# Kernel tuning notes

Hardware: AMD Instinct MI355X
Metric: run time of the kernel (lower is better)

The kernel has to match this reference:

```python
import jax, jax.numpy as jnp
import numpy as np

B, S, D = 2048, 8, 1280
K = 1                 # n_components_remove
HIGH_T = 0.6          # PC1_HIGH_ACTIVITY_THRESHOLD
STORM_T = 0.8         # solar_storm_threshold


def setup_inputs() -> dict:
    key = jax.random.key(0)
    k1, k2 = jax.random.split(key, 2)
    features = jax.random.normal(k1, (B, S, D), dtype=jnp.float32)
    kp_index = jax.random.uniform(k2, (B,), dtype=jnp.float32) * 9.0
    cmr_gate = jnp.ones((1,), dtype=jnp.float32)  # nn.Parameter(torch.ones(1))
    return {"features": features, "kp_index": kp_index, "cmr_gate": cmr_gate}


def reference(features, kp_index, cmr_gate):
    # Per-sample standardization over the feature axis (numpy std, ddof=0)
    mu = features.mean(axis=2, keepdims=True)            # (B, S, 1)
    sigma = features.std(axis=2, keepdims=True) + 1e-8   # (B, S, 1)
    fn = (features - mu) / sigma                         # (B, S, D)

    # Batched thin SVD of the (S, D) normalized feature matrix
    U, sv, Vt = jnp.linalg.svd(fn, full_matrices=False)  # (B,S,S), (B,S), (B,S,D)
    var = sv * sv
    pc1_ratio = var[:, 0] / (var.sum(axis=-1) + 1e-8)    # (B,)

    # solar_flag: 0 normal, 1 high activity, 2 storm
    solar_flag = (pc1_ratio >= HIGH_T).astype(jnp.int32) + (pc1_ratio >= STORM_T).astype(jnp.int32)

    # Rank-K reconstruction of the common-mode (solar) component
    low = jnp.einsum('bsk,bk,bkd->bsd', U[:, :, :K], sv[:, :K], Vt[:, :K, :])
    clean = (fn - low) * sigma + mu                      # de-normalized cleaned features

    # Kp-gating: amplify CMR when Kp >= 5
    kp_gate = 1.0 + 0.5 * (kp_index >= 5.0).astype(features.dtype)[:, None, None]
    clean = features + kp_gate * (clean - features)

    # Learnable gate
    gate = jax.nn.sigmoid(cmr_gate)[0]
    features_clean = features + gate * (clean - features)
    return features_clean, pc1_ratio, solar_flag
```

## Files before the change

### kernel.cpp

```cpp
#include <hip/hip_runtime.h>
#include <math.h>


#define SV 8
#define DV 1280
#define BSTRIDE (SV*DV)
#define WSS 17

__global__ __launch_bounds__(256)
void cmr_stats_kernel(const float* __restrict__ feat,
                      const float* __restrict__ kp,
                      const float* __restrict__ cmr_gate,
                      float* __restrict__ cws,
                      float* __restrict__ out,
                      int Bn)
{
    const int lane = threadIdx.x & 63;
    const int b = blockIdx.x * 4 + (threadIdx.x >> 6);

    const float* __restrict__ fb = feat + (size_t)b * BSTRIDE;

    float Sr[8], C[36];
#pragma unroll
    for (int s = 0; s < 8; ++s) Sr[s] = 0.f;
#pragma unroll
    for (int t = 0; t < 36; ++t) C[t] = 0.f;

#pragma unroll
    for (int k = 0; k < DV / 64; ++k) {
        const int d = lane + 64 * k;
        float f[8];
#pragma unroll
        for (int s = 0; s < 8; ++s) f[s] = fb[s * DV + d];
#pragma unroll
        for (int s = 0; s < 8; ++s) Sr[s] += f[s];
        int idx = 0;
#pragma unroll
        for (int i = 0; i < 8; ++i)
#pragma unroll
            for (int j = i; j < 8; ++j) { C[idx] = fmaf(f[i], f[j], C[idx]); ++idx; }
    }
#pragma unroll
    for (int m = 32; m >= 1; m >>= 1) {
#pragma unroll
        for (int s = 0; s < 8; ++s) Sr[s] += __shfl_xor(Sr[s], m);
#pragma unroll
        for (int t = 0; t < 36; ++t) C[t] += __shfl_xor(C[t], m);
    }

    const int i = lane >> 3, j = lane & 7;
    const int a_ = (i < j) ? i : j;
    const int b_ = (i < j) ? j : i;
    const int tii = 8 * i - (i * (i - 1)) / 2;
    const int tjj = 8 * j - (j * (j - 1)) / 2;
    const int tij = 8 * a_ - (a_ * (a_ - 1)) / 2 + (b_ - a_);

    float Ci = 0.f, Cj = 0.f, Cij = 0.f, Si = 0.f, Sj = 0.f;
#pragma unroll
    for (int t = 0; t < 36; ++t) {
        Ci  = (t == tii) ? C[t] : Ci;
        Cj  = (t == tjj) ? C[t] : Cj;
        Cij = (t == tij) ? C[t] : Cij;
    }
#pragma unroll
    for (int s = 0; s < 8; ++s) {
        Si = (s == i) ? Sr[s] : Si;
        Sj = (s == j) ? Sr[s] : Sj;
    }
    const float invD = 1.f / (float)DV;
    const float mui = Si * invD, muj = Sj * invD;
    const float vari = fmaxf(Ci * invD - mui * mui, 0.f);
    const float varj = fmaxf(Cj * invD - muj * muj, 0.f);
    const float sigi = sqrtf(vari) + 1e-8f;
    const float sigj = sqrtf(varj) + 1e-8f;
    const float rsigi = 1.f / sigi, rsigj = 1.f / sigj;
    const float G = ((Cij - (float)DV * mui * muj) * rsigi) * rsigj;

    float tr = (i == j) ? G : 0.f;
#pragma unroll
    for (int m = 32; m >= 1; m >>= 1) tr += __shfl_xor(tr, m);
    const float trs = fmaxf(tr, 1e-30f);

    float A = G / trs;
#pragma unroll
    for (int t = 0; t < 14; ++t) {
        float nb = 0.f;
#pragma unroll
        for (int k = 0; k < 8; ++k)
            nb = fmaf(__shfl(A, i * 8 + k), __shfl(A, k * 8 + j), nb);
        float dg = (i == j) ? nb : 0.f;
#pragma unroll
        for (int m = 32; m >= 1; m >>= 1) dg += __shfl_xor(dg, m);
        A = nb / fmaxf(dg, 1e-30f);
    }

    float dv = (i == j) ? A : -1.f;
    int bj = j;
#pragma unroll
    for (int m = 32; m >= 1; m >>= 1) {
        float ov = __shfl_xor(dv, m);
        int   oj = __shfl_xor(bj, m);
        if (ov > dv) { dv = ov; bj = oj; }
    }
    float u = __shfl(A, i * 8 + bj);
    {
        float nn = (j == 0) ? u * u : 0.f;
#pragma unroll
        for (int m = 32; m >= 1; m >>= 1) nn += __shfl_xor(nn, m);
        u *= rsqrtf(fmaxf(nn, 1e-30f));
    }
#pragma unroll
    for (int it = 0; it < 2; ++it) {
        float y = G * __shfl(u, j * 8);
#pragma unroll
        for (int m = 1; m <= 4; m <<= 1) y += __shfl_xor(y, m);
        float ny = (j == 0) ? y * y : 0.f;
#pragma unroll
        for (int m = 32; m >= 1; m >>= 1) ny += __shfl_xor(ny, m);
        u = y * rsqrtf(fmaxf(ny, 1e-30f));
    }
    float lp = G * u * __shfl(u, j * 8);
#pragma unroll
    for (int m = 32; m >= 1; m >>= 1) lp += __shfl_xor(lp, m);
    const float pc1 = lp / (tr + 1e-8f);

    const float gate = 1.f / (1.f + expf(-cmr_gate[0]));
    const float kpg  = (kp[b] >= 5.0f) ? 1.5f : 1.0f;
    const float Gt   = gate * kpg;

    float bcp = (j == 0) ? u * rsigi * mui : 0.f;
#pragma unroll
    for (int m = 32; m >= 1; m >>= 1) bcp += __shfl_xor(bcp, m);

    float* wsb = cws + (size_t)b * WSS;
    if (j == 0) {
        wsb[i]     = u * rsigi;
        wsb[8 + i] = Gt * sigi * u;
    }
    if (lane == 0) {
        wsb[16] = bcp;
        out[(size_t)Bn * BSTRIDE + b] = pc1;
        const float flag = (pc1 >= 0.6f ? 1.f : 0.f) + (pc1 >= 0.8f ? 1.f : 0.f);
        out[(size_t)Bn * BSTRIDE + Bn + b] = flag;
    }
}

__global__ __launch_bounds__(256)
void cmr_apply_kernel(const float* __restrict__ feat,
                      const float* __restrict__ cws,
                      float* __restrict__ out)
{
    const int lane = threadIdx.x & 63;
    const int b = blockIdx.x * 4 + (threadIdx.x >> 6);

    const float* __restrict__ wsb = cws + (size_t)b * WSS;
    float a[8], c[8];
#pragma unroll
    for (int s = 0; s < 8; ++s) { a[s] = wsb[s]; c[s] = wsb[8 + s]; }
    const float bc = wsb[16];

    const float4* __restrict__ f4 = (const float4*)(feat + (size_t)b * BSTRIDE);
    float4* __restrict__ o4 = (float4*)(out + (size_t)b * BSTRIDE);

#pragma unroll
    for (int k = 0; k < 5; ++k) {
        const int d4 = lane + 64 * k;
        float4 f[8];
#pragma unroll
        for (int s = 0; s < 8; ++s) f[s] = f4[s * (DV / 4) + d4];
        float4 p = make_float4(-bc, -bc, -bc, -bc);
#pragma unroll
        for (int s = 0; s < 8; ++s) {
            p.x = fmaf(a[s], f[s].x, p.x);
            p.y = fmaf(a[s], f[s].y, p.y);
            p.z = fmaf(a[s], f[s].z, p.z);
            p.w = fmaf(a[s], f[s].w, p.w);
        }
#pragma unroll
        for (int s = 0; s < 8; ++s) {
            float4 o;
            o.x = fmaf(-c[s], p.x, f[s].x);
            o.y = fmaf(-c[s], p.y, f[s].y);
            o.z = fmaf(-c[s], p.z, f[s].z);
            o.w = fmaf(-c[s], p.w, f[s].w);
            o4[s * (DV / 4) + d4] = o;
        }
    }
}

extern "C" void kernel_launch(void* const* d_in, const int* in_sizes, int n_in,
                              void* d_out, int out_size, void* d_ws, size_t ws_size,
                              hipStream_t stream) {
    const float* feat = (const float*)d_in[0];
    const float* kp   = (const float*)d_in[1];
    const float* gate = (const float*)d_in[2];
    float* out = (float*)d_out;
    float* cws = (float*)d_ws;
    const int Bn = in_sizes[0] / BSTRIDE;

    cmr_stats_kernel<<<Bn / 4, 256, 0, stream>>>(feat, kp, gate, cws, out, Bn);
    cmr_apply_kernel<<<Bn / 4, 256, 0, stream>>>(feat, cws, out);
}
```

Measured before the change: 179.8 us.

## Fuse stats and apply kernels, keeping each sample's features in registers

Merges the statistics and apply kernels into one kernel. Each wavefront loads its whole 8x1280 sample as float4 into registers (160 floats per lane), computes the Gram/power-iteration statistics, then applies the rank-1 removal from those same registers. This drops the second global read of the features and the workspace round trip. In exchange, register pressure is very high (launch_bounds 256,2), which can cause spills and lowers occupancy, so there is less latency hiding during the single big load phase.

```diff
diff --git a/kernel.cpp b/kernel.cpp
--- a/kernel.cpp
+++ b/kernel.cpp
@@ -4,41 +4,47 @@
 
 #define SV 8
 #define DV 1280
+#define D4 (DV/4)
 #define BSTRIDE (SV*DV)
-#define WSS 17
 
-__global__ __launch_bounds__(256)
-void cmr_stats_kernel(const float* __restrict__ feat,
+__global__ __launch_bounds__(256, 2)
+void cmr_fused_kernel(const float* __restrict__ feat,
                       const float* __restrict__ kp,
                       const float* __restrict__ cmr_gate,
-                      float* __restrict__ cws,
                       float* __restrict__ out,
                       int Bn)
 {
     const int lane = threadIdx.x & 63;
     const int b = blockIdx.x * 4 + (threadIdx.x >> 6);
 
-    const float* __restrict__ fb = feat + (size_t)b * BSTRIDE;
+    const float4* __restrict__ f4 = (const float4*)(feat + (size_t)b * BSTRIDE);
+    float4 f[8][5];
+#pragma unroll
+    for (int k = 0; k < 5; ++k) {
+        const int d4 = lane + 64 * k;
+#pragma unroll
+        for (int s = 0; s < 8; ++s) f[s][k] = f4[s * D4 + d4];
+    }
 
     float Sr[8], C[36];
 #pragma unroll
     for (int s = 0; s < 8; ++s) Sr[s] = 0.f;
 #pragma unroll
     for (int t = 0; t < 36; ++t) C[t] = 0.f;
-
 #pragma unroll
-    for (int k = 0; k < DV / 64; ++k) {
-        const int d = lane + 64 * k;
-        float f[8];
+    for (int k = 0; k < 5; ++k) {
 #pragma unroll
-        for (int s = 0; s < 8; ++s) f[s] = fb[s * DV + d];
-#pragma unroll
-        for (int s = 0; s < 8; ++s) Sr[s] += f[s];
+        for (int s = 0; s < 8; ++s)
+            Sr[s] += (f[s][k].x + f[s][k].y) + (f[s][k].z + f[s][k].w);
         int idx = 0;
 #pragma unroll
         for (int i = 0; i < 8; ++i)
 #pragma unroll
-            for (int j = i; j < 8; ++j) { C[idx] = fmaf(f[i], f[j], C[idx]); ++idx; }
+            for (int j = i; j < 8; ++j) {
+                float t0 = fmaf(f[i][k].x, f[j][k].x, fmaf(f[i][k].y, f[j][k].y, 0.f));
+                float t1 = fmaf(f[i][k].z, f[j][k].z, fmaf(f[i][k].w, f[j][k].w, t0));
+                C[idx] += t1; ++idx;
+            }
     }
 #pragma unroll
     for (int m = 32; m >= 1; m >>= 1) {
@@ -72,8 +78,8 @@
     const float vari = fmaxf(Ci * invD - mui * mui, 0.f);
     const float varj = fmaxf(Cj * invD - muj * muj, 0.f);
     const float sigi = sqrtf(vari) + 1e-8f;
-    const float sigj = sqrtf(varj) + 1e-8f;
-    const float rsigi = 1.f / sigi, rsigj = 1.f / sigj;
+    const float rsigi = 1.f / sigi;
+    const float rsigj = 1.f / (sqrtf(varj) + 1e-8f);
     const float G = ((Cij - (float)DV * mui * muj) * rsigi) * rsigj;
 
     float tr = (i == j) ? G : 0.f;
@@ -93,7 +99,6 @@
         for (int m = 32; m >= 1; m >>= 1) dg += __shfl_xor(dg, m);
         A = nb / fmaxf(dg, 1e-30f);
     }
-
     float dv = (i == j) ? A : -1.f;
     int bj = j;
 #pragma unroll
@@ -128,63 +133,46 @@
     const float kpg  = (kp[b] >= 5.0f) ? 1.5f : 1.0f;
     const float Gt   = gate * kpg;
 
-    float bcp = (j == 0) ? u * rsigi * mui : 0.f;
+    float bc = (j == 0) ? u * rsigi * mui : 0.f;
 #pragma unroll
-    for (int m = 32; m >= 1; m >>= 1) bcp += __shfl_xor(bcp, m);
+    for (int m = 32; m >= 1; m >>= 1) bc += __shfl_xor(bc, m);
 
-    float* wsb = cws + (size_t)b * WSS;
-    if (j == 0) {
-        wsb[i]     = u * rsigi;
-        wsb[8 + i] = Gt * sigi * u;
-    }
-    if (lane == 0) {
-        wsb[16] = bcp;
-        out[(size_t)Bn * BSTRIDE + b] = pc1;
-        const float flag = (pc1 >= 0.6f ? 1.f : 0.f) + (pc1 >= 0.8f ? 1.f : 0.f);
-        out[(size_t)Bn * BSTRIDE + Bn + b] = flag;
-    }
-}
-
-__global__ __launch_bounds__(256)
-void cmr_apply_kernel(const float* __restrict__ feat,
-                      const float* __restrict__ cws,
-                      float* __restrict__ out)
-{
-    const int lane = threadIdx.x & 63;
-    const int b = blockIdx.x * 4 + (threadIdx.x >> 6);
-
-    const float* __restrict__ wsb = cws + (size_t)b * WSS;
+    const float av = u * rsigi;
+    const float cv = Gt * sigi * u;
     float a[8], c[8];
 #pragma unroll
-    for (int s = 0; s < 8; ++s) { a[s] = wsb[s]; c[s] = wsb[8 + s]; }
-    const float bc = wsb[16];
+    for (int s = 0; s < 8; ++s) {
+        a[s] = __shfl(av, s * 8);
+        c[s] = __shfl(cv, s * 8);
+    }
 
-    const float4* __restrict__ f4 = (const float4*)(feat + (size_t)b * BSTRIDE);
     float4* __restrict__ o4 = (float4*)(out + (size_t)b * BSTRIDE);
-
 #pragma unroll
     for (int k = 0; k < 5; ++k) {
         const int d4 = lane + 64 * k;
-        float4 f[8];
-#pragma unroll
-        for (int s = 0; s < 8; ++s) f[s] = f4[s * (DV / 4) + d4];
         float4 p = make_float4(-bc, -bc, -bc, -bc);
 #pragma unroll
         for (int s = 0; s < 8; ++s) {
-            p.x = fmaf(a[s], f[s].x, p.x);
-            p.y = fmaf(a[s], f[s].y, p.y);
-            p.z = fmaf(a[s], f[s].z, p.z);
-            p.w = fmaf(a[s], f[s].w, p.w);
+            p.x = fmaf(a[s], f[s][k].x, p.x);
+            p.y = fmaf(a[s], f[s][k].y, p.y);
+            p.z = fmaf(a[s], f[s][k].z, p.z);
+            p.w = fmaf(a[s], f[s][k].w, p.w);
         }
 #pragma unroll
         for (int s = 0; s < 8; ++s) {
             float4 o;
-            o.x = fmaf(-c[s], p.x, f[s].x);
-            o.y = fmaf(-c[s], p.y, f[s].y);
-            o.z = fmaf(-c[s], p.z, f[s].z);
-            o.w = fmaf(-c[s], p.w, f[s].w);
-            o4[s * (DV / 4) + d4] = o;
+            o.x = fmaf(-c[s], p.x, f[s][k].x);
+            o.y = fmaf(-c[s], p.y, f[s][k].y);
+            o.z = fmaf(-c[s], p.z, f[s][k].z);
+            o.w = fmaf(-c[s], p.w, f[s][k].w);
+            o4[s * D4 + d4] = o;
         }
+    }
+
+    if (lane == 0) {
+        out[(size_t)Bn * BSTRIDE + b] = pc1;
+        const float flag = (pc1 >= 0.6f ? 1.f : 0.f) + (pc1 >= 0.8f ? 1.f : 0.f);
+        out[(size_t)Bn * BSTRIDE + Bn + b] = flag;
     }
 }
 
@@ -194,10 +182,6 @@
     const float* feat = (const float*)d_in[0];
     const float* kp   = (const float*)d_in[1];
     const float* gate = (const float*)d_in[2];
-    float* out = (float*)d_out;
-    float* cws = (float*)d_ws;
     const int Bn = in_sizes[0] / BSTRIDE;
-
-    cmr_stats_kernel<<<Bn / 4, 256, 0, stream>>>(feat, kp, gate, cws, out, Bn);
-    cmr_apply_kernel<<<Bn / 4, 256, 0, stream>>>(feat, cws, out);
+    cmr_fused_kernel<<<Bn / 4, 256, 0, stream>>>(feat, kp, gate, (float*)d_out, Bn);
 }
```

Measured after the change: 249.0 us. +38.4%, slower.

## Use one 320-thread block per sample with LDS cross-wave Gram reduction

Applied to the files above, without the earlier changes.

Both kernels now map one block of five waves to each batch sample instead of one wave per sample. In the stats kernel each thread loads float4s once, computes partial sums and Gram entries, reduces within 8-lane groups, and combines the 40 partials through shared memory. Wave 0 then does the power-iteration eigensolve, with the wide butterfly reductions replaced by direct diagonal-lane shuffles. The aim is more memory-level parallelism and vectorized loads in the bandwidth-bound stats pass, at the cost of a block barrier and four of the five waves sitting idle during the eigen step.

```diff
diff --git a/kernel.cpp b/kernel.cpp
--- a/kernel.cpp
+++ b/kernel.cpp
@@ -4,48 +4,75 @@
 
 #define SV 8
 #define DV 1280
+#define D4 320
 #define BSTRIDE (SV*DV)
+#define LDW 44
 #define WSS 17
 
-__global__ __launch_bounds__(256)
-void cmr_stats_kernel(const float* __restrict__ feat,
-                      const float* __restrict__ kp,
-                      const float* __restrict__ cmr_gate,
-                      float* __restrict__ cws,
-                      float* __restrict__ out,
-                      int Bn)
+__global__ __launch_bounds__(320)
+void cmr_stats(const float* __restrict__ feat,
+               const float* __restrict__ kp,
+               const float* __restrict__ cmr_gate,
+               float* __restrict__ cws,
+               float* __restrict__ out,
+               int Bn)
 {
-    const int lane = threadIdx.x & 63;
-    const int b = blockIdx.x * 4 + (threadIdx.x >> 6);
-
-    const float* __restrict__ fb = feat + (size_t)b * BSTRIDE;
+    __shared__ float lds[44 * LDW];
+    const int tid  = threadIdx.x;
+    const int lane = tid & 63;
+    const int wq   = tid >> 6;
+    const int b    = blockIdx.x;
+
+    const float4* __restrict__ f4 = (const float4*)(feat + (size_t)b * BSTRIDE);
+    const int d4 = wq * 64 + lane;
+    float4 f[8];
+#pragma unroll
+    for (int s = 0; s < 8; ++s) f[s] = f4[s * D4 + d4];
 
     float Sr[8], C[36];
 #pragma unroll
-    for (int s = 0; s < 8; ++s) Sr[s] = 0.f;
-#pragma unroll
-    for (int t = 0; t < 36; ++t) C[t] = 0.f;
-
-#pragma unroll
-    for (int k = 0; k < DV / 64; ++k) {
-        const int d = lane + 64 * k;
-        float f[8];
-#pragma unroll
-        for (int s = 0; s < 8; ++s) f[s] = fb[s * DV + d];
-#pragma unroll
-        for (int s = 0; s < 8; ++s) Sr[s] += f[s];
+    for (int s = 0; s < 8; ++s) Sr[s] = (f[s].x + f[s].y) + (f[s].z + f[s].w);
+    {
         int idx = 0;
 #pragma unroll
-        for (int i = 0; i < 8; ++i)
-#pragma unroll
-            for (int j = i; j < 8; ++j) { C[idx] = fmaf(f[i], f[j], C[idx]); ++idx; }
-    }
-#pragma unroll
-    for (int m = 32; m >= 1; m >>= 1) {
+        for (int i2 = 0; i2 < 8; ++i2)
+#pragma unroll
+            for (int j2 = i2; j2 < 8; ++j2) {
+                float t0 = fmaf(f[i2].x, f[j2].x, fmaf(f[i2].y, f[j2].y, 0.f));
+                C[idx] = fmaf(f[i2].z, f[j2].z, fmaf(f[i2].w, f[j2].w, t0));
+                ++idx;
+            }
+    }
+#pragma unroll
+    for (int m = 1; m <= 4; m <<= 1) {
 #pragma unroll
         for (int s = 0; s < 8; ++s) Sr[s] += __shfl_xor(Sr[s], m);
 #pragma unroll
         for (int t = 0; t < 36; ++t) C[t] += __shfl_xor(C[t], m);
+    }
+    {
+        const int p = wq * 8 + (lane >> 3);
+        if ((lane & 7) == 0) {
+#pragma unroll
+            for (int t = 0; t < 36; ++t) lds[t * LDW + p] = C[t];
+#pragma unroll
+            for (int s = 0; s < 8; ++s) lds[(36 + s) * LDW + p] = Sr[s];
+        }
+    }
+    __syncthreads();
+    if (wq != 0) return;
+
+    float tot;
+    {
+        const float4* l4 = (const float4*)lds;
+        const int Lr = (lane < 44) ? lane : 0;
+        float4 a4 = make_float4(0.f, 0.f, 0.f, 0.f);
+#pragma unroll
+        for (int q = 0; q < 10; ++q) {
+            float4 v = l4[Lr * (LDW / 4) + q];
+            a4.x += v.x; a4.y += v.y; a4.z += v.z; a4.w += v.w;
+        }
+        tot = (a4.x + a4.y) + (a4.z + a4.w);
     }
 
     const int i = lane >> 3, j = lane & 7;
@@ -54,83 +81,75 @@
     const int tii = 8 * i - (i * (i - 1)) / 2;
     const int tjj = 8 * j - (j * (j - 1)) / 2;
     const int tij = 8 * a_ - (a_ * (a_ - 1)) / 2 + (b_ - a_);
-
-    float Ci = 0.f, Cj = 0.f, Cij = 0.f, Si = 0.f, Sj = 0.f;
-#pragma unroll
-    for (int t = 0; t < 36; ++t) {
-        Ci  = (t == tii) ? C[t] : Ci;
-        Cj  = (t == tjj) ? C[t] : Cj;
-        Cij = (t == tij) ? C[t] : Cij;
-    }
-#pragma unroll
-    for (int s = 0; s < 8; ++s) {
-        Si = (s == i) ? Sr[s] : Si;
-        Sj = (s == j) ? Sr[s] : Sj;
-    }
+    const float Cij = __shfl(tot, tij);
+    const float Ci  = __shfl(tot, tii);
+    const float Cj  = __shfl(tot, tjj);
+    const float Si  = __shfl(tot, 36 + i);
+    const float Sj  = __shfl(tot, 36 + j);
+
     const float invD = 1.f / (float)DV;
     const float mui = Si * invD, muj = Sj * invD;
     const float vari = fmaxf(Ci * invD - mui * mui, 0.f);
     const float varj = fmaxf(Cj * invD - muj * muj, 0.f);
-    const float sigi = sqrtf(vari) + 1e-8f;
-    const float sigj = sqrtf(varj) + 1e-8f;
-    const float rsigi = 1.f / sigi, rsigj = 1.f / sigj;
+    const float sigi  = sqrtf(vari) + 1e-8f;
+    const float rsigi = 1.f / sigi;
+    const float rsigj = 1.f / (sqrtf(varj) + 1e-8f);
     const float G = ((Cij - (float)DV * mui * muj) * rsigi) * rsigj;
 
-    float tr = (i == j) ? G : 0.f;
-#pragma unroll
-    for (int m = 32; m >= 1; m >>= 1) tr += __shfl_xor(tr, m);
-    const float trs = fmaxf(tr, 1e-30f);
-
-    float A = G / trs;
+    float tr = 0.f;
+#pragma unroll
+    for (int k = 0; k < 8; ++k) tr += __shfl(G, 9 * k);
+
+    float A = G / fmaxf(tr, 1e-30f);
 #pragma unroll
     for (int t = 0; t < 14; ++t) {
         float nb = 0.f;
 #pragma unroll
         for (int k = 0; k < 8; ++k)
             nb = fmaf(__shfl(A, i * 8 + k), __shfl(A, k * 8 + j), nb);
-        float dg = (i == j) ? nb : 0.f;
-#pragma unroll
-        for (int m = 32; m >= 1; m >>= 1) dg += __shfl_xor(dg, m);
+        float dg = 0.f;
+#pragma unroll
+        for (int k = 0; k < 8; ++k) dg += __shfl(nb, 9 * k);
         A = nb / fmaxf(dg, 1e-30f);
     }
-
-    float dv = (i == j) ? A : -1.f;
-    int bj = j;
-#pragma unroll
-    for (int m = 32; m >= 1; m >>= 1) {
-        float ov = __shfl_xor(dv, m);
-        int   oj = __shfl_xor(bj, m);
-        if (ov > dv) { dv = ov; bj = oj; }
+    float best = __shfl(A, 0); int bj = 0;
+#pragma unroll
+    for (int k = 1; k < 8; ++k) {
+        float dk = __shfl(A, 9 * k);
+        if (dk > best) { best = dk; bj = k; }
     }
     float u = __shfl(A, i * 8 + bj);
     {
-        float nn = (j == 0) ? u * u : 0.f;
-#pragma unroll
-        for (int m = 32; m >= 1; m >>= 1) nn += __shfl_xor(nn, m);
+        float nn = 0.f;
+#pragma unroll
+        for (int k = 0; k < 8; ++k) nn += __shfl(u * u, 9 * k);
         u *= rsqrtf(fmaxf(nn, 1e-30f));
     }
 #pragma unroll
     for (int it = 0; it < 2; ++it) {
-        float y = G * __shfl(u, j * 8);
+        float y = G * __shfl(u, 9 * j);
 #pragma unroll
         for (int m = 1; m <= 4; m <<= 1) y += __shfl_xor(y, m);
-        float ny = (j == 0) ? y * y : 0.f;
-#pragma unroll
-        for (int m = 32; m >= 1; m >>= 1) ny += __shfl_xor(ny, m);
+        float ny = 0.f;
+#pragma unroll
+        for (int k = 0; k < 8; ++k) ny += __shfl(y * y, 9 * k);
         u = y * rsqrtf(fmaxf(ny, 1e-30f));
     }
-    float lp = G * u * __shfl(u, j * 8);
-#pragma unroll
-    for (int m = 32; m >= 1; m >>= 1) lp += __shfl_xor(lp, m);
-    const float pc1 = lp / (tr + 1e-8f);
+    float v = G * u * __shfl(u, 9 * j);
+#pragma unroll
+    for (int m = 1; m <= 4; m <<= 1) v += __shfl_xor(v, m);
+    float lam = 0.f;
+#pragma unroll
+    for (int k = 0; k < 8; ++k) lam += __shfl(v, 9 * k);
+    const float pc1 = lam / (tr + 1e-8f);
 
     const float gate = 1.f / (1.f + expf(-cmr_gate[0]));
     const float kpg  = (kp[b] >= 5.0f) ? 1.5f : 1.0f;
     const float Gt   = gate * kpg;
 
-    float bcp = (j == 0) ? u * rsigi * mui : 0.f;
-#pragma unroll
-    for (int m = 32; m >= 1; m >>= 1) bcp += __shfl_xor(bcp, m);
+    float bc = 0.f;
+#pragma unroll
+    for (int k = 0; k < 8; ++k) bc += __shfl(u * rsigi * mui, 9 * k);
 
     float* wsb = cws + (size_t)b * WSS;
     if (j == 0) {
@@ -138,20 +157,22 @@
         wsb[8 + i] = Gt * sigi * u;
     }
     if (lane == 0) {
-        wsb[16] = bcp;
+        wsb[16] = bc;
         out[(size_t)Bn * BSTRIDE + b] = pc1;
         const float flag = (pc1 >= 0.6f ? 1.f : 0.f) + (pc1 >= 0.8f ? 1.f : 0.f);
         out[(size_t)Bn * BSTRIDE + Bn + b] = flag;
     }
 }
 
-__global__ __launch_bounds__(256)
-void cmr_apply_kernel(const float* __restrict__ feat,
-                      const float* __restrict__ cws,
-                      float* __restrict__ out)
+__global__ __launch_bounds__(320)
+void cmr_apply(const float* __restrict__ feat,
+               const float* __restrict__ cws,
+               float* __restrict__ out)
 {
-    const int lane = threadIdx.x & 63;
-    const int b = blockIdx.x * 4 + (threadIdx.x >> 6);
+    const int tid  = threadIdx.x;
+    const int lane = tid & 63;
+    const int wq   = tid >> 6;
+    const int b    = blockIdx.x;
 
     const float* __restrict__ wsb = cws + (size_t)b * WSS;
     float a[8], c[8];
@@ -161,30 +182,28 @@
 
     const float4* __restrict__ f4 = (const float4*)(feat + (size_t)b * BSTRIDE);
     float4* __restrict__ o4 = (float4*)(out + (size_t)b * BSTRIDE);
-
-#pragma unroll
-    for (int k = 0; k < 5; ++k) {
-        const int d4 = lane + 64 * k;
-        float4 f[8];
-#pragma unroll
-        for (int s = 0; s < 8; ++s) f[s] = f4[s * (DV / 4) + d4];
-        float4 p = make_float4(-bc, -bc, -bc, -bc);
-#pragma unroll
-        for (int s = 0; s < 8; ++s) {
-            p.x = fmaf(a[s], f[s].x, p.x);
-            p.y = fmaf(a[s], f[s].y, p.y);
-            p.z = fmaf(a[s], f[s].z, p.z);
-            p.w = fmaf(a[s], f[s].w, p.w);
-        }
-#pragma unroll
-        for (int s = 0; s < 8; ++s) {
-            float4 o;
-            o.x = fmaf(-c[s], p.x, f[s].x);
-            o.y = fmaf(-c[s], p.y, f[s].y);
-            o.z = fmaf(-c[s], p.z, f[s].z);
-            o.w = fmaf(-c[s], p.w, f[s].w);
-            o4[s * (DV / 4) + d4] = o;
-        }
+    const int d4 = wq * 64 + lane;
+
+    float4 f[8];
+#pragma unroll
+    for (int s = 0; s < 8; ++s) f[s] = f4[s * D4 + d4];
+
+    float4 p = make_float4(-bc, -bc, -bc, -bc);
+#pragma unroll
+    for (int s = 0; s < 8; ++s) {
+        p.x = fmaf(a[s], f[s].x, p.x);
+        p.y = fmaf(a[s], f[s].y, p.y);
+        p.z = fmaf(a[s], f[s].z, p.z);
+        p.w = fmaf(a[s], f[s].w, p.w);
+    }
+#pragma unroll
+    for (int s = 0; s < 8; ++s) {
+        float4 o;
+        o.x = fmaf(-c[s], p.x, f[s].x);
+        o.y = fmaf(-c[s], p.y, f[s].y);
+        o.z = fmaf(-c[s], p.z, f[s].z);
+        o.w = fmaf(-c[s], p.w, f[s].w);
+        o4[s * D4 + d4] = o;
     }
 }
 
@@ -198,6 +217,6 @@
     float* cws = (float*)d_ws;
     const int Bn = in_sizes[0] / BSTRIDE;
 
-    cmr_stats_kernel<<<Bn / 4, 256, 0, stream>>>(feat, kp, gate, cws, out, Bn);
-    cmr_apply_kernel<<<Bn / 4, 256, 0, stream>>>(feat, cws, out);
+    cmr_stats<<<Bn, 320, 0, stream>>>(feat, kp, gate, cws, out, Bn);
+    cmr_apply<<<Bn, 320, 0, stream>>>(feat, cws, out);
 }
```

New measurement: 177.1 us. About the same (-1.5%).
